# Optimization experiments

Measured on AMD Instinct MI355X. Metric: run time of the kernel, lower is better.

Reference implementation:

```python
import jax, jax.numpy as jnp
import numpy as np

N = 100000   # nodes per node type
E = 300000   # edges per relation
HID = 128
HEADS = 2
C = HID // HEADS  # 64 per-head channels
IN = 16
NEG_SLOPE = 0.2


def _gatv2(x_src, x_dst, ei, Wl, Wr, att, b):
    """PyG GATv2Conv, add_self_loops=False, share_weights=False, concat heads."""
    n_dst = x_dst.shape[0]
    src, dst = ei[0], ei[1]
    gl = (x_src @ Wl).reshape(-1, HEADS, C)[src]   # [E,H,C] gathered source messages
    gr = (x_dst @ Wr).reshape(-1, HEADS, C)[dst]   # [E,H,C]
    e = jnp.einsum('ehc,hc->eh', jax.nn.leaky_relu(gl + gr, NEG_SLOPE), att)  # [E,H]
    emax = jax.ops.segment_max(e, dst, num_segments=n_dst)       # per-dst max (softmax stability)
    p = jnp.exp(e - emax[dst])
    denom = jax.ops.segment_sum(p, dst, num_segments=n_dst)
    alpha = p / (denom[dst] + 1e-16)                              # scatter-softmax
    out = jax.ops.segment_sum(alpha[..., None] * gl, dst, num_segments=n_dst)
    return out.reshape(n_dst, HEADS * C) + b


def _hetero_layer(ht, hv, he, eis, Wl, Wr, att, bc):
    # relation order: 0 t->t, 1 t->v, 2 v->t, 3 t->e, 4 e->t, 5 v->e, 6 e->v, 7 v->v, 8 e->e
    g = lambda i, xs, xd: _gatv2(xs, xd, eis[i], Wl[i], Wr[i], att[i], bc[i])
    ot = g(0, ht, ht) + g(2, hv, ht) + g(4, he, ht)   # aggr='sum' over dst=tile
    ov = g(1, ht, hv) + g(6, he, hv) + g(7, hv, hv)   # dst=vertex
    oe = g(3, ht, he) + g(5, hv, he) + g(8, he, he)   # dst=edge
    return ot, ov, oe


def setup_inputs() -> dict:
    key = jax.random.key(0)
    ks = jax.random.split(key, 32)
    d = {
        'xt': jax.random.normal(ks[0], (N, IN), jnp.float32),
        'xv': jax.random.normal(ks[1], (N, IN), jnp.float32),
        'xe': jax.random.normal(ks[2], (N, IN), jnp.float32),
    }
    names = ['ei_tt', 'ei_tv', 'ei_vt', 'ei_te', 'ei_et', 'ei_ve', 'ei_ev', 'ei_vv', 'ei_ee']
    for i, nm in enumerate(names):
        d[nm] = jax.random.randint(ks[3 + i], (2, E), 0, N, dtype=jnp.int32)
    s_in = 1.0 / np.sqrt(IN)
    s_h = 1.0 / np.sqrt(HID)
    for j, t in enumerate(['t', 'v', 'e']):
        d[f'W{t}'] = jax.random.uniform(ks[12 + j], (IN, HID), jnp.float32, -s_in, s_in)
        d[f'b{t}'] = jax.random.uniform(ks[15 + j], (HID,), jnp.float32, -s_in, s_in)
    for l in (1, 2):
        o = 18 + (l - 1) * 4
        d[f'Wl{l}'] = jax.random.uniform(ks[o], (9, HID, HID), jnp.float32, -s_h, s_h)
        d[f'Wr{l}'] = jax.random.uniform(ks[o + 1], (9, HID, HID), jnp.float32, -s_h, s_h)
        d[f'att{l}'] = jax.random.uniform(ks[o + 2], (9, HEADS, C), jnp.float32, -s_h, s_h)
        d[f'bc{l}'] = jnp.zeros((9, HID), jnp.float32)
    return d


def reference(xt, xv, xe, ei_tt, ei_tv, ei_vt, ei_te, ei_et, ei_ve, ei_ev, ei_vv, ei_ee,
              Wt, bt, Wv, bv, We, be, Wl1, Wr1, att1, bc1, Wl2, Wr2, att2, bc2):
    eis = [ei_tt, ei_tv, ei_vt, ei_te, ei_et, ei_ve, ei_ev, ei_vv, ei_ee]
    ht = xt @ Wt + bt  # in_proj per node type
    hv = xv @ Wv + bv
    he = xe @ We + be
    ht, hv, he = _hetero_layer(ht, hv, he, eis, Wl1, Wr1, att1, bc1)
    ht, hv, he = jax.nn.relu(ht), jax.nn.relu(hv), jax.nn.relu(he)
    ht, hv, he = _hetero_layer(ht, hv, he, eis, Wl2, Wr2, att2, bc2)
    return jnp.concatenate([ht, hv, he], axis=0)  # [3N, HID]
```

## Files before the change

kernel.cpp:

```cpp
#include <hip/hip_runtime.h>


#define NN 100000
#define NE 300000
#define NH (NN * 128)
#define NB 391

typedef __attribute__((ext_vector_type(8))) short short8;
typedef __attribute__((ext_vector_type(4))) float f32x4;

__device__ __forceinline__ float bf2f(unsigned short h) {
    return __uint_as_float(((unsigned)h) << 16);
}
__device__ __forceinline__ unsigned short f2bf(float x) {
    unsigned u = __float_as_uint(x);
    return (unsigned short)((u + 0x7FFFu + ((u >> 16) & 1u)) >> 16);
}

struct EPtrs { const int* p[9]; };
struct G6 { const unsigned short* A[6]; const float* W[6]; unsigned short* O[6]; };
struct GatA {
    const unsigned short* PL[3];
    const unsigned short* PR[3];
    const int* rowp[3];
    const int* csrc[3];
    const float* att[3];
    const float* bias[3];
};

__global__ void inproj_k(const float* __restrict__ X, const float* __restrict__ W,
                         const float* __restrict__ b, unsigned short* __restrict__ H, int M) {
    int w = (int)((blockIdx.x * blockDim.x + threadIdx.x) >> 6);
    int lane = threadIdx.x & 63;
    if (w >= M) return;
    const float* x = X + (long)w * 16;
    float a0 = 0.f, a1 = 0.f;
#pragma unroll
    for (int k = 0; k < 16; ++k) {
        float xv = x[k];
        a0 = fmaf(xv, W[k * 128 + lane], a0);
        a1 = fmaf(xv, W[k * 128 + 64 + lane], a1);
    }
    H[(long)w * 128 + lane] = f2bf(a0 + b[lane]);
    H[(long)w * 128 + 64 + lane] = f2bf(a1 + b[64 + lane]);
}

__global__ __launch_bounds__(256) void gemm6_k(G6 g, int M) {
    __shared__ unsigned short Bt[128 * 136];
    int which = blockIdx.y;
    const unsigned short* A = g.A[which];
    const float* W = g.W[which];
    unsigned short* O = g.O[which];
    int tid = threadIdx.x;
#pragma unroll
    for (int i = 0; i < 64; ++i) {
        int idx = i * 256 + tid;
        int k = idx >> 7, c = idx & 127;
        Bt[c * 136 + k] = f2bf(W[idx]);
    }
    __syncthreads();
    int wv = tid >> 6, lane = tid & 63;
    int quad = lane >> 4, l15 = lane & 15;
    long rowbase = (long)blockIdx.x * 64 + wv * 16;
    long arow = rowbase + l15;
    if (arow > M - 1) arow = M - 1;
    f32x4 acc[8];
#pragma unroll
    for (int n = 0; n < 8; ++n) acc[n] = (f32x4){0.f, 0.f, 0.f, 0.f};
#pragma unroll
    for (int kb = 0; kb < 4; ++kb) {
        short8 a = *(const short8*)(A + arow * 128 + kb * 32 + quad * 8);
#pragma unroll
        for (int n = 0; n < 8; ++n) {
            short8 b = *(const short8*)(&Bt[(n * 16 + l15) * 136 + kb * 32 + quad * 8]);
            acc[n] = __builtin_amdgcn_mfma_f32_16x16x32_bf16(a, b, acc[n], 0, 0, 0);
        }
    }
#pragma unroll
    for (int n = 0; n < 8; ++n)
#pragma unroll
        for (int r = 0; r < 4; ++r) {
            long row = rowbase + quad * 4 + r;
            if (row < M) O[row * 128 + n * 16 + l15] = f2bf(acc[n][r]);
        }
}

__global__ void count_k(EPtrs ep, int* __restrict__ deg) {
    int r = blockIdx.y;
    int e = blockIdx.x * 256 + threadIdx.x;
    if (e >= NE) return;
    atomicAdd(&deg[r * NN + ep.p[r][NE + e]], 1);
}

__global__ void scanA_k(const int* __restrict__ deg, int* __restrict__ bsum) {
    __shared__ int sm[256];
    int r = blockIdx.y, b = blockIdx.x, t = threadIdx.x;
    int i = b * 256 + t;
    sm[t] = (i < NN) ? deg[r * NN + i] : 0;
    __syncthreads();
#pragma unroll
    for (int o = 128; o; o >>= 1) {
        if (t < o) sm[t] += sm[t + o];
        __syncthreads();
    }
    if (t == 0) bsum[r * NB + b] = sm[0];
}

__global__ void scanB_k(int* __restrict__ bsum) {
    __shared__ int sm[512];
    int r = blockIdx.x, t = threadIdx.x;
    int v = (t < NB) ? bsum[r * NB + t] : 0;
    sm[t] = v;
    __syncthreads();
    for (int o = 1; o < 512; o <<= 1) {
        int x = (t >= o) ? sm[t - o] : 0;
        __syncthreads();
        sm[t] += x;
        __syncthreads();
    }
    if (t < NB) bsum[r * NB + t] = sm[t] - v;
}

__global__ void scanC_k(int* __restrict__ deg, const int* __restrict__ bsum,
                        int* __restrict__ rowp) {
    __shared__ int sm[256];
    int r = blockIdx.y, b = blockIdx.x, t = threadIdx.x;
    int i = b * 256 + t;
    int v = (i < NN) ? deg[r * NN + i] : 0;
    sm[t] = v;
    __syncthreads();
    for (int o = 1; o < 256; o <<= 1) {
        int x = (t >= o) ? sm[t - o] : 0;
        __syncthreads();
        sm[t] += x;
        __syncthreads();
    }
    int excl = sm[t] - v + bsum[r * NB + b];
    if (i < NN) {
        rowp[r * (NN + 1) + i] = excl;
        deg[r * NN + i] = excl;
        if (i == NN - 1) rowp[r * (NN + 1) + NN] = excl + v;
    }
}

__global__ void scat_k(EPtrs ep, int* __restrict__ cursor, int* __restrict__ csrc) {
    int r = blockIdx.y;
    int e = blockIdx.x * 256 + threadIdx.x;
    if (e >= NE) return;
    int s = ep.p[r][e], d = ep.p[r][NE + e];
    int pos = atomicAdd(&cursor[r * NN + d], 1);
    csrc[(long)r * NE + pos] = s;
}

__global__ void gat3_k(GatA g, float* __restrict__ outF, unsigned short* __restrict__ outH,
                       int mode) {
    int w = (int)((blockIdx.x * blockDim.x + threadIdx.x) >> 6);
    int c = threadIdx.x & 63;
    if (w >= NN) return;
    float acc0 = 0.f, acc1 = 0.f;
#pragma unroll
    for (int j = 0; j < 3; ++j) {
        const unsigned short* PL = g.PL[j];
        float gr0 = bf2f(g.PR[j][(long)w * 128 + c]);
        float gr1 = bf2f(g.PR[j][(long)w * 128 + 64 + c]);
        float at0 = g.att[j][c], at1 = g.att[j][64 + c];
        int beg = g.rowp[j][w], end = g.rowp[j][w + 1];
        float m0 = -1e30f, m1 = -1e30f, s0 = 0.f, s1 = 0.f, a0 = 0.f, a1 = 0.f;
        for (int i = beg; i < end; ++i) {
            int s = g.csrc[j][i];
            float gl0 = bf2f(PL[(long)s * 128 + c]);
            float gl1 = bf2f(PL[(long)s * 128 + 64 + c]);
            float v0 = gl0 + gr0;
            v0 = (v0 > 0.f ? v0 : 0.2f * v0) * at0;
            float v1 = gl1 + gr1;
            v1 = (v1 > 0.f ? v1 : 0.2f * v1) * at1;
#pragma unroll
            for (int o = 32; o; o >>= 1) {
                v0 += __shfl_xor(v0, o);
                v1 += __shfl_xor(v1, o);
            }
            float mn0 = fmaxf(m0, v0), sc0 = __expf(m0 - mn0), p0 = __expf(v0 - mn0);
            s0 = s0 * sc0 + p0; a0 = a0 * sc0 + p0 * gl0; m0 = mn0;
            float mn1 = fmaxf(m1, v1), sc1 = __expf(m1 - mn1), p1 = __expf(v1 - mn1);
            s1 = s1 * sc1 + p1; a1 = a1 * sc1 + p1 * gl1; m1 = mn1;
        }
        acc0 += a0 / (s0 + 1e-16f) + g.bias[j][c];
        acc1 += a1 / (s1 + 1e-16f) + g.bias[j][64 + c];
    }
    long o = (long)w * 128 + c;
    if (mode == 0) {
        outH[o] = f2bf(fmaxf(acc0, 0.f));
        outH[o + 64] = f2bf(fmaxf(acc1, 0.f));
    } else {
        outF[o] = acc0;
        outF[o + 64] = acc1;
    }
}

__global__ void sentinel_k(float* out) { out[0] = 123456.0f; }

extern "C" void kernel_launch(void* const* d_in, const int* in_sizes, int n_in,
                              void* d_out, int out_size, void* d_ws, size_t ws_size,
                              hipStream_t stream) {
    const float* xin[3] = {(const float*)d_in[0], (const float*)d_in[1], (const float*)d_in[2]};
    EPtrs ep;
    for (int r = 0; r < 9; ++r) ep.p[r] = (const int*)d_in[3 + r];
    const float* Win[3] = {(const float*)d_in[12], (const float*)d_in[14], (const float*)d_in[16]};
    const float* bin[3] = {(const float*)d_in[13], (const float*)d_in[15], (const float*)d_in[17]};
    const float* Wl[2] = {(const float*)d_in[18], (const float*)d_in[22]};
    const float* Wr[2] = {(const float*)d_in[19], (const float*)d_in[23]};
    const float* att[2] = {(const float*)d_in[20], (const float*)d_in[24]};
    const float* bc[2] = {(const float*)d_in[21], (const float*)d_in[25]};

    size_t nInt = (size_t)9 * NN + (size_t)9 * NB + (size_t)9 * (NN + 1) + (size_t)9 * NE;
    size_t need = (size_t)12 * NH * 2 + nInt * 4;
    if (ws_size < need) {
        hipMemsetAsync(d_out, 0, (size_t)out_size * 4, stream);
        sentinel_k<<<1, 1, 0, stream>>>((float*)d_out);
        return;
    }
    unsigned short* h1 = (unsigned short*)d_ws;
    unsigned short* h2 = h1 + (size_t)3 * NH;
    unsigned short* pl = h2 + (size_t)3 * NH;
    unsigned short* pr = pl + (size_t)3 * NH;
    int* deg = (int*)(pr + (size_t)3 * NH);
    int* bsum = deg + (size_t)9 * NN;
    int* rowp = bsum + (size_t)9 * NB;
    int* csrc = rowp + (size_t)9 * (NN + 1);

    static const int ST[9] = {0, 0, 1, 0, 2, 1, 2, 1, 2};
    static const int RT[3][3] = {{0, 2, 4}, {1, 6, 7}, {3, 5, 8}};

    for (int T = 0; T < 3; ++T)
        inproj_k<<<NN / 4, 256, 0, stream>>>(xin[T], Win[T], bin[T], h1 + (size_t)T * NH, NN);

    hipMemsetAsync(deg, 0, (size_t)9 * NN * 4, stream);
    dim3 eg((NE + 255) / 256, 9), ng(NB, 9);
    count_k<<<eg, 256, 0, stream>>>(ep, deg);
    scanA_k<<<ng, 256, 0, stream>>>(deg, bsum);
    scanB_k<<<9, 512, 0, stream>>>(bsum);
    scanC_k<<<ng, 256, 0, stream>>>(deg, bsum, rowp);
    scat_k<<<eg, 256, 0, stream>>>(ep, deg, csrc);

    dim3 gg((NN + 63) / 64, 6);
    for (int l = 0; l < 2; ++l) {
        unsigned short* hc = (l == 0) ? h1 : h2;
        for (int T = 0; T < 3; ++T) {
            G6 g6;
            GatA ga;
            for (int j = 0; j < 3; ++j) {
                int r = RT[T][j];
                g6.A[j] = hc + (size_t)ST[r] * NH;
                g6.W[j] = Wl[l] + (size_t)r * 16384;
                g6.O[j] = pl + (size_t)j * NH;
                g6.A[3 + j] = hc + (size_t)T * NH;
                g6.W[3 + j] = Wr[l] + (size_t)r * 16384;
                g6.O[3 + j] = pr + (size_t)j * NH;
                ga.PL[j] = pl + (size_t)j * NH;
                ga.PR[j] = pr + (size_t)j * NH;
                ga.rowp[j] = rowp + (size_t)r * (NN + 1);
                ga.csrc[j] = csrc + (size_t)r * NE;
                ga.att[j] = att[l] + (size_t)r * 128;
                ga.bias[j] = bc[l] + (size_t)r * 128;
            }
            gemm6_k<<<gg, 256, 0, stream>>>(g6, NN);
            if (l == 0)
                gat3_k<<<NN / 4, 256, 0, stream>>>(ga, nullptr, h2 + (size_t)T * NH, 0);
            else
                gat3_k<<<NN / 4, 256, 0, stream>>>(ga, (float*)d_out + (size_t)T * NH, nullptr, 1);
        }
    }
}
```

Before: 2.040 ms.

## Split fused GAT kernel into per-edge score, softmax, and aggregation passes

The fused per-destination wavefront kernel did a serial online softmax with a 64-lane shuffle reduction on every edge. It is replaced by three kernels: a thread-per-edge score kernel that computes the dot product over 128 channels, a per-node softmax pass over the CSR rows, and a lean aggregation kernel with packed bf16 reads and writes. Weights are also pre-transposed to bf16 once, so the GEMM blocks no longer rebuild a shared-memory tile. The cost is extra launches, extra global traffic for the score and denominator arrays, and a serial per-thread softmax loop.

```diff
diff --git a/kernel.cpp b/kernel.cpp
--- a/kernel.cpp
+++ b/kernel.cpp
@@ -18,13 +18,23 @@
 }
 
 struct EPtrs { const int* p[9]; };
-struct G6 { const unsigned short* A[6]; const float* W[6]; unsigned short* O[6]; };
-struct GatA {
+struct G6 { const unsigned short* A[6]; const unsigned short* WT[6]; unsigned short* O[6]; };
+struct W4 { const float* in[4]; unsigned short* out[4]; };
+struct ScoA {
     const unsigned short* PL[3];
     const unsigned short* PR[3];
+    const int* csrc[3];
+    const int* cdst[3];
+    const float* att[3];
+    float2* esc[3];
+};
+struct SfmA { const int* rowp[3]; float2* esc[3]; float2* denom[3]; };
+struct AggA {
+    const unsigned short* PL[3];
     const int* rowp[3];
     const int* csrc[3];
-    const float* att[3];
+    const float2* alpha[3];
+    const float2* denom[3];
     const float* bias[3];
 };
 
@@ -45,20 +55,25 @@
     H[(long)w * 128 + 64 + lane] = f2bf(a1 + b[64 + lane]);
 }
 
+__global__ void wcvt_k(W4 w) {
+    int b = blockIdx.x;
+    int a = b / 9, r = b % 9;
+    const float* in = w.in[a] + (long)r * 16384;
+    unsigned short* out = w.out[a] + (long)r * 16384;
+#pragma unroll 4
+    for (int it = 0; it < 64; ++it) {
+        int idx = it * 256 + threadIdx.x;
+        int k = idx >> 7, n = idx & 127;
+        out[n * 128 + k] = f2bf(in[idx]);
+    }
+}
+
 __global__ __launch_bounds__(256) void gemm6_k(G6 g, int M) {
-    __shared__ unsigned short Bt[128 * 136];
     int which = blockIdx.y;
     const unsigned short* A = g.A[which];
-    const float* W = g.W[which];
+    const unsigned short* WT = g.WT[which];
     unsigned short* O = g.O[which];
     int tid = threadIdx.x;
-#pragma unroll
-    for (int i = 0; i < 64; ++i) {
-        int idx = i * 256 + tid;
-        int k = idx >> 7, c = idx & 127;
-        Bt[c * 136 + k] = f2bf(W[idx]);
-    }
-    __syncthreads();
     int wv = tid >> 6, lane = tid & 63;
     int quad = lane >> 4, l15 = lane & 15;
     long rowbase = (long)blockIdx.x * 64 + wv * 16;
@@ -72,7 +87,7 @@
         short8 a = *(const short8*)(A + arow * 128 + kb * 32 + quad * 8);
 #pragma unroll
         for (int n = 0; n < 8; ++n) {
-            short8 b = *(const short8*)(&Bt[(n * 16 + l15) * 136 + kb * 32 + quad * 8]);
+            short8 b = *(const short8*)(WT + (n * 16 + l15) * 128 + kb * 32 + quad * 8);
             acc[n] = __builtin_amdgcn_mfma_f32_16x16x32_bf16(a, b, acc[n], 0, 0, 0);
         }
     }
@@ -143,57 +158,100 @@
     }
 }
 
-__global__ void scat_k(EPtrs ep, int* __restrict__ cursor, int* __restrict__ csrc) {
+__global__ void scat_k(EPtrs ep, int* __restrict__ cursor, int* __restrict__ csrc,
+                       int* __restrict__ cdst) {
     int r = blockIdx.y;
     int e = blockIdx.x * 256 + threadIdx.x;
     if (e >= NE) return;
     int s = ep.p[r][e], d = ep.p[r][NE + e];
     int pos = atomicAdd(&cursor[r * NN + d], 1);
     csrc[(long)r * NE + pos] = s;
-}
-
-__global__ void gat3_k(GatA g, float* __restrict__ outF, unsigned short* __restrict__ outH,
-                       int mode) {
+    cdst[(long)r * NE + pos] = d;
+}
+
+__global__ void score_k(ScoA g) {
+    int j = blockIdx.y;
+    int i = blockIdx.x * 256 + threadIdx.x;
+    if (i >= NE) return;
+    int s = g.csrc[j][i], d = g.cdst[j][i];
+    const unsigned short* pls = g.PL[j] + (long)s * 128;
+    const unsigned short* prd = g.PR[j] + (long)d * 128;
+    const float* att = g.att[j];
+    float e0a = 0.f, e0b = 0.f, e1a = 0.f, e1b = 0.f;
+#pragma unroll
+    for (int kb = 0; kb < 16; ++kb) {
+        short8 a = *(const short8*)(pls + kb * 8);
+        short8 b = *(const short8*)(prd + kb * 8);
+#pragma unroll
+        for (int u = 0; u < 8; ++u) {
+            float x = bf2f((unsigned short)a[u]) + bf2f((unsigned short)b[u]);
+            float lv = fmaxf(x, 0.f) + 0.2f * fminf(x, 0.f);
+            float av = att[kb * 8 + u];
+            if (kb < 8) {
+                if (u & 1) e0b = fmaf(lv, av, e0b); else e0a = fmaf(lv, av, e0a);
+            } else {
+                if (u & 1) e1b = fmaf(lv, av, e1b); else e1a = fmaf(lv, av, e1a);
+            }
+        }
+    }
+    g.esc[j][i] = make_float2(e0a + e0b, e1a + e1b);
+}
+
+__global__ void sfm_k(SfmA g) {
+    int j = blockIdx.y;
+    int t = blockIdx.x * 256 + threadIdx.x;
+    if (t >= NN) return;
+    int beg = g.rowp[j][t], end = g.rowp[j][t + 1];
+    float2* e = g.esc[j];
+    float m0 = -1e30f, m1 = -1e30f;
+    for (int i = beg; i < end; ++i) {
+        float2 v = e[i];
+        m0 = fmaxf(m0, v.x);
+        m1 = fmaxf(m1, v.y);
+    }
+    float s0 = 0.f, s1 = 0.f;
+    for (int i = beg; i < end; ++i) {
+        float2 v = e[i];
+        float p0 = __expf(v.x - m0), p1 = __expf(v.y - m1);
+        s0 += p0;
+        s1 += p1;
+        e[i] = make_float2(p0, p1);
+    }
+    g.denom[j][t] = make_float2(s0, s1);
+}
+
+__global__ void agg_k(AggA g, float* __restrict__ outF, unsigned short* __restrict__ outH,
+                      int mode) {
     int w = (int)((blockIdx.x * blockDim.x + threadIdx.x) >> 6);
-    int c = threadIdx.x & 63;
+    int l = threadIdx.x & 63;
     if (w >= NN) return;
-    float acc0 = 0.f, acc1 = 0.f;
+    float accx = 0.f, accy = 0.f;
 #pragma unroll
     for (int j = 0; j < 3; ++j) {
         const unsigned short* PL = g.PL[j];
-        float gr0 = bf2f(g.PR[j][(long)w * 128 + c]);
-        float gr1 = bf2f(g.PR[j][(long)w * 128 + 64 + c]);
-        float at0 = g.att[j][c], at1 = g.att[j][64 + c];
+        const int* cs = g.csrc[j];
+        const float2* al = g.alpha[j];
         int beg = g.rowp[j][w], end = g.rowp[j][w + 1];
-        float m0 = -1e30f, m1 = -1e30f, s0 = 0.f, s1 = 0.f, a0 = 0.f, a1 = 0.f;
+        float ax = 0.f, ay = 0.f;
         for (int i = beg; i < end; ++i) {
-            int s = g.csrc[j][i];
-            float gl0 = bf2f(PL[(long)s * 128 + c]);
-            float gl1 = bf2f(PL[(long)s * 128 + 64 + c]);
-            float v0 = gl0 + gr0;
-            v0 = (v0 > 0.f ? v0 : 0.2f * v0) * at0;
-            float v1 = gl1 + gr1;
-            v1 = (v1 > 0.f ? v1 : 0.2f * v1) * at1;
-#pragma unroll
-            for (int o = 32; o; o >>= 1) {
-                v0 += __shfl_xor(v0, o);
-                v1 += __shfl_xor(v1, o);
-            }
-            float mn0 = fmaxf(m0, v0), sc0 = __expf(m0 - mn0), p0 = __expf(v0 - mn0);
-            s0 = s0 * sc0 + p0; a0 = a0 * sc0 + p0 * gl0; m0 = mn0;
-            float mn1 = fmaxf(m1, v1), sc1 = __expf(m1 - mn1), p1 = __expf(v1 - mn1);
-            s1 = s1 * sc1 + p1; a1 = a1 * sc1 + p1 * gl1; m1 = mn1;
-        }
-        acc0 += a0 / (s0 + 1e-16f) + g.bias[j][c];
-        acc1 += a1 / (s1 + 1e-16f) + g.bias[j][64 + c];
-    }
-    long o = (long)w * 128 + c;
+            int s = cs[i];
+            float2 p = al[i];
+            float pv = (l < 32) ? p.x : p.y;
+            unsigned gg = *(const unsigned*)(PL + (long)s * 128 + 2 * l);
+            ax = fmaf(pv, bf2f((unsigned short)(gg & 0xffffu)), ax);
+            ay = fmaf(pv, bf2f((unsigned short)(gg >> 16)), ay);
+        }
+        float2 dn = g.denom[j][w];
+        float inv = 1.f / (((l < 32) ? dn.x : dn.y) + 1e-16f);
+        accx += ax * inv + g.bias[j][2 * l];
+        accy += ay * inv + g.bias[j][2 * l + 1];
+    }
     if (mode == 0) {
-        outH[o] = f2bf(fmaxf(acc0, 0.f));
-        outH[o + 64] = f2bf(fmaxf(acc1, 0.f));
+        unsigned px = (unsigned)f2bf(fmaxf(accx, 0.f)) |
+                      ((unsigned)f2bf(fmaxf(accy, 0.f)) << 16);
+        *(unsigned*)(outH + (long)w * 128 + 2 * l) = px;
     } else {
-        outF[o] = acc0;
-        outF[o + 64] = acc1;
+        *(float2*)(outF + (long)w * 128 + 2 * l) = make_float2(accx, accy);
     }
 }
 
@@ -212,8 +270,9 @@
     const float* att[2] = {(const float*)d_in[20], (const float*)d_in[24]};
     const float* bc[2] = {(const float*)d_in[21], (const float*)d_in[25]};
 
-    size_t nInt = (size_t)9 * NN + (size_t)9 * NB + (size_t)9 * (NN + 1) + (size_t)9 * NE;
-    size_t need = (size_t)12 * NH * 2 + nInt * 4;
+    size_t nInt = (size_t)9 * NN + (size_t)9 * NB + (size_t)9 * (NN + 1) + (size_t)18 * NE;
+    size_t nF = (size_t)3 * NE * 2 + (size_t)3 * NN * 2;
+    size_t need = ((size_t)12 * NH + 589824) * 2 + nF * 4 + nInt * 4;
     if (ws_size < need) {
         hipMemsetAsync(d_out, 0, (size_t)out_size * 4, stream);
         sentinel_k<<<1, 1, 0, stream>>>((float*)d_out);
@@ -223,16 +282,27 @@
     unsigned short* h2 = h1 + (size_t)3 * NH;
     unsigned short* pl = h2 + (size_t)3 * NH;
     unsigned short* pr = pl + (size_t)3 * NH;
-    int* deg = (int*)(pr + (size_t)3 * NH);
+    unsigned short* wT = pr + (size_t)3 * NH;
+    float2* esc = (float2*)(wT + 589824);
+    float2* denomp = esc + (size_t)3 * NE;
+    int* deg = (int*)(denomp + (size_t)3 * NN);
     int* bsum = deg + (size_t)9 * NN;
     int* rowp = bsum + (size_t)9 * NB;
     int* csrc = rowp + (size_t)9 * (NN + 1);
+    int* cdst = csrc + (size_t)9 * NE;
 
     static const int ST[9] = {0, 0, 1, 0, 2, 1, 2, 1, 2};
     static const int RT[3][3] = {{0, 2, 4}, {1, 6, 7}, {3, 5, 8}};
 
     for (int T = 0; T < 3; ++T)
         inproj_k<<<NN / 4, 256, 0, stream>>>(xin[T], Win[T], bin[T], h1 + (size_t)T * NH, NN);
+
+    {
+        W4 w4;
+        w4.in[0] = Wl[0]; w4.in[1] = Wr[0]; w4.in[2] = Wl[1]; w4.in[3] = Wr[1];
+        for (int a = 0; a < 4; ++a) w4.out[a] = wT + (size_t)a * 9 * 16384;
+        wcvt_k<<<36, 256, 0, stream>>>(w4);
+    }
 
     hipMemsetAsync(deg, 0, (size_t)9 * NN * 4, stream);
     dim3 eg((NE + 255) / 256, 9), ng(NB, 9);
@@ -240,34 +310,45 @@
     scanA_k<<<ng, 256, 0, stream>>>(deg, bsum);
     scanB_k<<<9, 512, 0, stream>>>(bsum);
     scanC_k<<<ng, 256, 0, stream>>>(deg, bsum, rowp);
-    scat_k<<<eg, 256, 0, stream>>>(ep, deg, csrc);
+    scat_k<<<eg, 256, 0, stream>>>(ep, deg, csrc, cdst);
 
     dim3 gg((NN + 63) / 64, 6);
+    dim3 sg((NE + 255) / 256, 3), fg((NN + 255) / 256, 3);
     for (int l = 0; l < 2; ++l) {
         unsigned short* hc = (l == 0) ? h1 : h2;
         for (int T = 0; T < 3; ++T) {
-            G6 g6;
-            GatA ga;
+            G6 g6; ScoA sc; SfmA sf; AggA ag;
             for (int j = 0; j < 3; ++j) {
                 int r = RT[T][j];
                 g6.A[j] = hc + (size_t)ST[r] * NH;
-                g6.W[j] = Wl[l] + (size_t)r * 16384;
+                g6.WT[j] = wT + (size_t)(l * 2 + 0) * 9 * 16384 + (size_t)r * 16384;
                 g6.O[j] = pl + (size_t)j * NH;
                 g6.A[3 + j] = hc + (size_t)T * NH;
-                g6.W[3 + j] = Wr[l] + (size_t)r * 16384;
+                g6.WT[3 + j] = wT + (size_t)(l * 2 + 1) * 9 * 16384 + (size_t)r * 16384;
                 g6.O[3 + j] = pr + (size_t)j * NH;
-                ga.PL[j] = pl + (size_t)j * NH;
-                ga.PR[j] = pr + (size_t)j * NH;
-                ga.rowp[j] = rowp + (size_t)r * (NN + 1);
-                ga.csrc[j] = csrc + (size_t)r * NE;
-                ga.att[j] = att[l] + (size_t)r * 128;
-                ga.bias[j] = bc[l] + (size_t)r * 128;
+                sc.PL[j] = pl + (size_t)j * NH;
+                sc.PR[j] = pr + (size_t)j * NH;
+                sc.csrc[j] = csrc + (size_t)r * NE;
+                sc.cdst[j] = cdst + (size_t)r * NE;
+                sc.att[j] = att[l] + (size_t)r * 128;
+                sc.esc[j] = esc + (size_t)j * NE;
+                sf.rowp[j] = rowp + (size_t)r * (NN + 1);
+                sf.esc[j] = esc + (size_t)j * NE;
+                sf.denom[j] = denomp + (size_t)j * NN;
+                ag.PL[j] = pl + (size_t)j * NH;
+                ag.rowp[j] = rowp + (size_t)r * (NN + 1);
+                ag.csrc[j] = csrc + (size_t)r * NE;
+                ag.alpha[j] = esc + (size_t)j * NE;
+                ag.denom[j] = denomp + (size_t)j * NN;
+                ag.bias[j] = bc[l] + (size_t)r * 128;
             }
             gemm6_k<<<gg, 256, 0, stream>>>(g6, NN);
+            score_k<<<sg, 256, 0, stream>>>(sc);
+            sfm_k<<<fg, 256, 0, stream>>>(sf);
             if (l == 0)
-                gat3_k<<<NN / 4, 256, 0, stream>>>(ga, nullptr, h2 + (size_t)T * NH, 0);
+                agg_k<<<NN / 4, 256, 0, stream>>>(ag, nullptr, h2 + (size_t)T * NH, 0);
             else
-                gat3_k<<<NN / 4, 256, 0, stream>>>(ga, (float*)d_out + (size_t)T * NH, nullptr, 1);
-        }
-    }
-}
+                agg_k<<<NN / 4, 256, 0, stream>>>(ag, (float*)d_out + (size_t)T * NH, nullptr, 1);
+        }
+    }
+}
```

After: 2.922 ms. +43.3%, slower.

## Remap GAT lanes to paired bf16 columns per head and shorten reductions

Applied to the files above, without the earlier changes.

Each lane now owns two adjacent channels of the same head: lanes 0-31 cover head 0 and lanes 32-63 cover head 1. Features are loaded as one 32-bit word and outputs are written as packed pairs. This halves the shuffle-reduction work, since there is one 5-step reduction instead of two 6-step ones, and it merges the two per-head online-softmax states into one. It also uses exp2 with log2e folded into the attention weights and readfirstlane on the edge source index, trading a small change in rounding for fewer instructions per edge.

```diff
diff --git a/kernel.cpp b/kernel.cpp
--- a/kernel.cpp
+++ b/kernel.cpp
@@ -5,6 +5,7 @@
 #define NE 300000
 #define NH (NN * 128)
 #define NB 391
+#define LOG2E 1.4426950408889634f
 
 typedef __attribute__((ext_vector_type(8))) short short8;
 typedef __attribute__((ext_vector_type(4))) float f32x4;
@@ -155,45 +156,53 @@
 __global__ void gat3_k(GatA g, float* __restrict__ outF, unsigned short* __restrict__ outH,
                        int mode) {
     int w = (int)((blockIdx.x * blockDim.x + threadIdx.x) >> 6);
-    int c = threadIdx.x & 63;
+    int l = threadIdx.x & 63;
     if (w >= NN) return;
+    int col = ((l >> 5) << 6) + ((l & 31) << 1);
     float acc0 = 0.f, acc1 = 0.f;
 #pragma unroll
     for (int j = 0; j < 3; ++j) {
         const unsigned short* PL = g.PL[j];
-        float gr0 = bf2f(g.PR[j][(long)w * 128 + c]);
-        float gr1 = bf2f(g.PR[j][(long)w * 128 + 64 + c]);
-        float at0 = g.att[j][c], at1 = g.att[j][64 + c];
+        unsigned grp = *(const unsigned*)(g.PR[j] + (long)w * 128 + col);
+        float gr0 = __uint_as_float(grp << 16);
+        float gr1 = __uint_as_float(grp & 0xffff0000u);
+        float at0 = g.att[j][col] * LOG2E;
+        float at1 = g.att[j][col + 1] * LOG2E;
         int beg = g.rowp[j][w], end = g.rowp[j][w + 1];
-        float m0 = -1e30f, m1 = -1e30f, s0 = 0.f, s1 = 0.f, a0 = 0.f, a1 = 0.f;
+        float m = -1e30f, sden = 0.f, a0 = 0.f, a1 = 0.f;
         for (int i = beg; i < end; ++i) {
-            int s = g.csrc[j][i];
-            float gl0 = bf2f(PL[(long)s * 128 + c]);
-            float gl1 = bf2f(PL[(long)s * 128 + 64 + c]);
-            float v0 = gl0 + gr0;
-            v0 = (v0 > 0.f ? v0 : 0.2f * v0) * at0;
-            float v1 = gl1 + gr1;
-            v1 = (v1 > 0.f ? v1 : 0.2f * v1) * at1;
-#pragma unroll
-            for (int o = 32; o; o >>= 1) {
-                v0 += __shfl_xor(v0, o);
-                v1 += __shfl_xor(v1, o);
-            }
-            float mn0 = fmaxf(m0, v0), sc0 = __expf(m0 - mn0), p0 = __expf(v0 - mn0);
-            s0 = s0 * sc0 + p0; a0 = a0 * sc0 + p0 * gl0; m0 = mn0;
-            float mn1 = fmaxf(m1, v1), sc1 = __expf(m1 - mn1), p1 = __expf(v1 - mn1);
-            s1 = s1 * sc1 + p1; a1 = a1 * sc1 + p1 * gl1; m1 = mn1;
-        }
-        acc0 += a0 / (s0 + 1e-16f) + g.bias[j][c];
-        acc1 += a1 / (s1 + 1e-16f) + g.bias[j][64 + c];
-    }
-    long o = (long)w * 128 + c;
+            int s = __builtin_amdgcn_readfirstlane(g.csrc[j][i]);
+            unsigned gg = *(const unsigned*)(PL + (long)s * 128 + col);
+            float gl0 = __uint_as_float(gg << 16);
+            float gl1 = __uint_as_float(gg & 0xffff0000u);
+            float x0 = gl0 + gr0, x1 = gl1 + gr1;
+            float t0 = fmaxf(x0, 0.f) + 0.2f * fminf(x0, 0.f);
+            float t1 = fmaxf(x1, 0.f) + 0.2f * fminf(x1, 0.f);
+            float v = t0 * at0 + t1 * at1;
+            v += __shfl_xor(v, 16);
+            v += __shfl_xor(v, 8);
+            v += __shfl_xor(v, 4);
+            v += __shfl_xor(v, 2);
+            v += __shfl_xor(v, 1);
+            float mn = fmaxf(m, v);
+            float sc = __builtin_exp2f(m - mn);
+            float p = __builtin_exp2f(v - mn);
+            sden = sden * sc + p;
+            a0 = a0 * sc + p * gl0;
+            a1 = a1 * sc + p * gl1;
+            m = mn;
+        }
+        float inv = 1.f / (sden + 1e-16f);
+        acc0 += a0 * inv + g.bias[j][col];
+        acc1 += a1 * inv + g.bias[j][col + 1];
+    }
+    long o = (long)w * 128 + col;
     if (mode == 0) {
-        outH[o] = f2bf(fmaxf(acc0, 0.f));
-        outH[o + 64] = f2bf(fmaxf(acc1, 0.f));
+        unsigned px = (unsigned)f2bf(fmaxf(acc0, 0.f)) |
+                      ((unsigned)f2bf(fmaxf(acc1, 0.f)) << 16);
+        *(unsigned*)(outH + o) = px;
     } else {
-        outF[o] = acc0;
-        outF[o + 64] = acc1;
+        *(float2*)(outF + o) = make_float2(acc0, acc1);
     }
 }
 
```

New measurement: 1.942 ms. 1.05x faster.
